# Kernel tuning notes

Hardware: AMD Instinct MI355X
Metric: run time of the kernel (lower is better)

Reference implementation:

```python
import jax, jax.numpy as jnp
import numpy as np

N, NFEAT, NHID, NHID2 = 10000, 512, 256, 128


def setup_inputs() -> dict:
    key = jax.random.key(0)
    k1, k2, k3, k4 = jax.random.split(key, 4)
    x = jax.random.normal(k1, (N, NFEAT), dtype=jnp.float32)
    # sparse-ish row-normalized adjacency, stored dense (as the module's spmm operand)
    raw = jax.random.uniform(k2, (N, N), dtype=jnp.float32)
    adj = jnp.where(raw > 0.995, raw, 0.0)
    adj = adj / jnp.maximum(adj.sum(axis=1, keepdims=True), 1e-6)
    W1 = jax.random.normal(k3, (NFEAT, NHID), dtype=jnp.float32) / np.sqrt(NFEAT)
    b1 = jnp.zeros((NHID,), dtype=jnp.float32)
    W2 = jax.random.normal(k4, (NHID, NHID2), dtype=jnp.float32) / np.sqrt(NHID)
    b2 = jnp.zeros((NHID2,), dtype=jnp.float32)
    return {"x": x, "adj": adj, "W1": W1, "b1": b1, "W2": W2, "b2": b2}


def gcn_conv(x, adj, W, b):
    # standard Kipf GCNConv: adj @ (x @ W) + b
    return adj @ (x @ W) + b


def reference(x, adj, W1, b1, W2, b2):
    h = jax.nn.relu(gcn_conv(x, adj, W1, b1))
    # dropout is identity in inference mode (training=False)
    h = jax.nn.relu(gcn_conv(h, adj, W2, b2))
    return h
```

## Files before the change

### kernel.cpp

```cpp
#include <hip/hip_runtime.h>

#define N_NODES 10000
#define NFEAT   512
#define NHID    256
#define NHID2   128
#define CAP     128

typedef __attribute__((ext_vector_type(8))) short bf16x8;
typedef __attribute__((ext_vector_type(4))) float f32x4;
typedef __attribute__((ext_vector_type(2))) int   i32x2;

__device__ __forceinline__ ushort f2bf(float f){
  union { float f; unsigned u; } v; v.f = f;
  unsigned r = v.u + 0x7FFFu + ((v.u >> 16) & 1u);
  return (ushort)(r >> 16);
}
__device__ __forceinline__ float bf2f(ushort u){
  union { unsigned u; float f; } v; v.u = ((unsigned)u) << 16; return v.f;
}

__global__ void k_cvt(const float* __restrict__ x, const float* __restrict__ W1,
                      const float* __restrict__ W2, ushort* __restrict__ xb,
                      ushort* __restrict__ w1t, ushort* __restrict__ w2t){
  const int b = blockIdx.x, t = threadIdx.x;
  if (b < 5000){
    int i = (b * 256 + t) * 4;
    float4 q = *(const float4*)(x + i);
    ushort4 o; o.x = f2bf(q.x); o.y = f2bf(q.y); o.z = f2bf(q.z); o.w = f2bf(q.w);
    *(ushort4*)(xb + i) = o;
  } else if (b < 5512){
    int id = (b - 5000) * 256 + t;
    int n = id >> 9, k = id & 511;
    w1t[id] = f2bf(W1[k * NHID + n]);
  } else {
    int id = (b - 5512) * 256 + t;
    int n = id >> 8, k = id & 255;
    w2t[id] = f2bf(W2[k * NHID2 + n]);
  }
}

__launch_bounds__(256)
__global__ void k_scan_gemm1(const float* __restrict__ adj, const ushort* __restrict__ xb,
                             const ushort* __restrict__ w1t, ushort* __restrict__ xw1_lo,
                             ushort* __restrict__ xw1_hi, int* __restrict__ row_nnz,
                             i32x2* __restrict__ pja){
  const int b = blockIdx.x, t = threadIdx.x;
  const int lane = t & 63, w = t >> 6;

  if (b < 628){
    const int bx = b % 157, by = b / 157;
    const int wr = w >> 1, wc = w & 1;
    const int r16 = lane & 15, kg = lane >> 4;
    const int row0 = bx * 64 + wr * 32;
    const int col0 = by * 64 + wc * 32;

    int arow[2], bcol[2];
    #pragma unroll
    for (int r = 0; r < 2; r++){
      int ar = row0 + r * 16 + r16;
      arow[r] = (ar >= N_NODES) ? (N_NODES - 1) : ar;
    }
    #pragma unroll
    for (int c = 0; c < 2; c++) bcol[c] = col0 + c * 16 + r16;

    f32x4 acc[2][2];
    #pragma unroll
    for (int r = 0; r < 2; r++)
      #pragma unroll
      for (int c = 0; c < 2; c++)
        acc[r][c] = (f32x4){0.f, 0.f, 0.f, 0.f};

    bf16x8 aA[2], bA[2], aB[2], bB[2];
    auto LOADF = [&](bf16x8* a, bf16x8* bb, int k0){
      #pragma unroll
      for (int r = 0; r < 2; r++)
        a[r] = *(const bf16x8*)(xb + (size_t)arow[r] * NFEAT + k0 + kg * 8);
      #pragma unroll
      for (int c = 0; c < 2; c++)
        bb[c] = *(const bf16x8*)(w1t + (size_t)bcol[c] * NFEAT + k0 + kg * 8);
    };
    auto MM = [&](bf16x8* a, bf16x8* bb){
      #pragma unroll
      for (int r = 0; r < 2; r++)
        #pragma unroll
        for (int c = 0; c < 2; c++)
          acc[r][c] = __builtin_amdgcn_mfma_f32_16x16x32_bf16(a[r], bb[c], acc[r][c], 0, 0, 0);
    };

    LOADF(aA, bA, 0);
    #pragma unroll
    for (int k0 = 0; k0 < NFEAT; k0 += 64){
      if (k0 + 32 < NFEAT) LOADF(aB, bB, k0 + 32);
      MM(aA, bA);
      if (k0 + 64 < NFEAT) LOADF(aA, bA, k0 + 64);
      if (k0 + 32 < NFEAT) MM(aB, bB);
    }

    ushort* dst = (by < 2) ? xw1_lo : xw1_hi;
    const int cbase = (by < 2) ? 0 : 128;
    #pragma unroll
    for (int r = 0; r < 2; r++)
      #pragma unroll
      for (int c = 0; c < 2; c++){
        int col = col0 + c * 16 + r16 - cbase;
        #pragma unroll
        for (int i = 0; i < 4; i++){
          int row = row0 + r * 16 + kg * 4 + i;
          if (row < N_NODES) dst[(size_t)row * 128 + col] = f2bf(acc[r][c][i]);
        }
      }
    return;
  }

  const int r = b - 628;
  const float* row = adj + (size_t)r * N_NODES;
  __shared__ int swave[4];

  f32x4 vals[10];
  #pragma unroll
  for (int v = 0; v < 9; v++)
    vals[v] = __builtin_nontemporal_load((const f32x4*)(row + v * 1024 + t * 4));
  vals[9] = (f32x4){0.f, 0.f, 0.f, 0.f};
  if (t < 196) vals[9] = __builtin_nontemporal_load((const f32x4*)(row + 9216 + t * 4));

  int cnt = 0;
  #pragma unroll
  for (int v = 0; v < 10; v++)
    cnt += (vals[v].x != 0.f) + (vals[v].y != 0.f) + (vals[v].z != 0.f) + (vals[v].w != 0.f);

  int incl = cnt;
  #pragma unroll
  for (int d = 1; d < 64; d <<= 1){
    int u = __shfl_up(incl, d, 64);
    if (lane >= d) incl += u;
  }
  if (lane == 63) swave[w] = incl;
  __syncthreads();
  int woff = 0, total = 0;
  #pragma unroll
  for (int i = 0; i < 4; i++){
    int s = swave[i];
    total += s;
    if (i < w) woff += s;
  }
  int pos = woff + incl - cnt;

  #pragma unroll
  for (int v = 0; v < 10; v++){
    float q[4] = {vals[v].x, vals[v].y, vals[v].z, vals[v].w};
    #pragma unroll
    for (int e = 0; e < 4; e++){
      if (q[e] != 0.f && pos < CAP){
        pja[(size_t)r * CAP + pos] = (i32x2){(v * 1024 + t * 4 + e) << 8, __float_as_int(q[e])};
        pos++;
      }
    }
  }
  if (t == 0) row_nnz[r] = min(total, CAP);
}

__launch_bounds__(256)
__global__ void k_agg1(const int* __restrict__ row_nnz, const i32x2* __restrict__ pja,
                       const ushort* __restrict__ xw1_lo, const ushort* __restrict__ xw1_hi,
                       const float* __restrict__ b1, ushort* __restrict__ Hb){
  const int half = blockIdx.x & 1;
  const int r0   = (blockIdx.x >> 1) * 16;
  const int t = threadIdx.x;
  __shared__ i32x2 sl[16][CAP];
  __shared__ int   sn[16];
  if (t < 16) sn[t] = row_nnz[r0 + t];
  #pragma unroll
  for (int e = 0; e < 8; e++){
    int idx = t + e * 256;
    int rr = idx >> 7, kk = idx & (CAP - 1);
    sl[rr][kk] = pja[(size_t)(r0 + rr) * CAP + kk];
  }
  __syncthreads();

  const int wv = t >> 6, lane = t & 63;
  const char* table = (const char*)(half ? xw1_hi : xw1_lo);
  const float bias0 = b1[half * 128 + lane * 2 + 0];
  const float bias1 = b1[half * 128 + lane * 2 + 1];

  #pragma unroll
  for (int rr = wv; rr < 16; rr += 4){
    const int n = sn[rr];
    float a0 = 0.f, a1 = 0.f;
    for (int k = 0; k < n; k++){
      i32x2 p = sl[rr][k];
      uint pk = *(const uint*)(table + p.x + lane * 4);
      float a = __int_as_float(p.y);
      a0 += a * bf2f((ushort)(pk & 0xffff));
      a1 += a * bf2f((ushort)(pk >> 16));
    }
    uint o = ((uint)f2bf(fmaxf(a1 + bias1, 0.f)) << 16) | (uint)f2bf(fmaxf(a0 + bias0, 0.f));
    *(uint*)(Hb + (size_t)(r0 + rr) * NHID + half * 128 + lane * 2) = o;
  }
}

__launch_bounds__(256)
__global__ void k_gemm2(const ushort* __restrict__ A, const ushort* __restrict__ Bt,
                        ushort* __restrict__ C){
  const int lane = threadIdx.x & 63;
  const int w    = threadIdx.x >> 6;
  const int wr   = w >> 1, wc = w & 1;
  const int r16  = lane & 15;
  const int kg   = lane >> 4;
  const int row0 = blockIdx.x * 64 + wr * 32;
  const int col0 = blockIdx.y * 64 + wc * 32;

  int arow[2], bcol[2];
  #pragma unroll
  for (int r = 0; r < 2; r++){
    int ar = row0 + r * 16 + r16;
    arow[r] = (ar >= N_NODES) ? (N_NODES - 1) : ar;
  }
  #pragma unroll
  for (int c = 0; c < 2; c++) bcol[c] = col0 + c * 16 + r16;

  f32x4 acc[2][2];
  #pragma unroll
  for (int r = 0; r < 2; r++)
    #pragma unroll
    for (int c = 0; c < 2; c++)
      acc[r][c] = (f32x4){0.f, 0.f, 0.f, 0.f};

  bf16x8 aA[2], bA[2], aB[2], bB[2];
  auto LOADF = [&](bf16x8* a, bf16x8* bb, int k0){
    #pragma unroll
    for (int r = 0; r < 2; r++)
      a[r] = *(const bf16x8*)(A + (size_t)arow[r] * NHID + k0 + kg * 8);
    #pragma unroll
    for (int c = 0; c < 2; c++)
      bb[c] = *(const bf16x8*)(Bt + (size_t)bcol[c] * NHID + k0 + kg * 8);
  };
  auto MM = [&](bf16x8* a, bf16x8* bb){
    #pragma unroll
    for (int r = 0; r < 2; r++)
      #pragma unroll
      for (int c = 0; c < 2; c++)
        acc[r][c] = __builtin_amdgcn_mfma_f32_16x16x32_bf16(a[r], bb[c], acc[r][c], 0, 0, 0);
  };

  LOADF(aA, bA, 0);
  #pragma unroll
  for (int k0 = 0; k0 < NHID; k0 += 64){
    if (k0 + 32 < NHID) LOADF(aB, bB, k0 + 32);
    MM(aA, bA);
    if (k0 + 64 < NHID) LOADF(aA, bA, k0 + 64);
    if (k0 + 32 < NHID) MM(aB, bB);
  }

  #pragma unroll
  for (int r = 0; r < 2; r++)
    #pragma unroll
    for (int c = 0; c < 2; c++){
      int col = col0 + c * 16 + r16;
      #pragma unroll
      for (int i = 0; i < 4; i++){
        int row = row0 + r * 16 + kg * 4 + i;
        if (row < N_NODES) C[(size_t)row * NHID2 + col] = f2bf(acc[r][c][i]);
      }
    }
}

__launch_bounds__(256)
__global__ void k_agg2(const int* __restrict__ row_nnz, const i32x2* __restrict__ pja,
                       const ushort* __restrict__ hw2b, const float* __restrict__ b2,
                       float* __restrict__ out){
  const int r0 = blockIdx.x * 8;
  const int t = threadIdx.x;
  __shared__ i32x2 sl[8][CAP];
  __shared__ int   sn[8];
  if (t < 8) sn[t] = row_nnz[r0 + t];
  #pragma unroll
  for (int e = 0; e < 4; e++){
    int idx = t + e * 256;
    int rr = idx >> 7, kk = idx & (CAP - 1);
    sl[rr][kk] = pja[(size_t)(r0 + rr) * CAP + kk];
  }
  __syncthreads();

  const int wv = t >> 6, lane = t & 63;
  const char* table = (const char*)hw2b;
  const float bias0 = b2[lane * 2 + 0];
  const float bias1 = b2[lane * 2 + 1];

  #pragma unroll
  for (int rr = wv; rr < 8; rr += 4){
    const int n = sn[rr];
    float a0 = 0.f, a1 = 0.f;
    for (int k = 0; k < n; k++){
      i32x2 p = sl[rr][k];
      uint pk = *(const uint*)(table + p.x + lane * 4);
      float a = __int_as_float(p.y);
      a0 += a * bf2f((ushort)(pk & 0xffff));
      a1 += a * bf2f((ushort)(pk >> 16));
    }
    float2 o = make_float2(fmaxf(a0 + bias0, 0.f), fmaxf(a1 + bias1, 0.f));
    *(float2*)(out + (size_t)(r0 + rr) * NHID2 + lane * 2) = o;
  }
}

extern "C" void kernel_launch(void* const* d_in, const int* in_sizes, int n_in,
                              void* d_out, int out_size, void* d_ws, size_t ws_size,
                              hipStream_t stream){
  const float* x   = (const float*)d_in[0];
  const float* adj = (const float*)d_in[1];
  const float* W1  = (const float*)d_in[2];
  const float* b1  = (const float*)d_in[3];
  const float* W2  = (const float*)d_in[4];
  const float* b2  = (const float*)d_in[5];
  float* out = (float*)d_out;
  char*  ws  = (char*)d_ws;

  ushort* xb     = (ushort*)(ws);
  ushort* w1t    = (ushort*)(ws + 10240000);
  ushort* w2t    = (ushort*)(ws + 10502144);
  ushort* xw1_lo = (ushort*)(ws + 10567680);
  ushort* xw1_hi = (ushort*)(ws + 13127680);
  ushort* Hb     = (ushort*)(ws + 15687680);
  ushort* hw2b   = (ushort*)(ws + 20807680);
  int*    nnz    = (int*)(ws + 23367680);
  i32x2*  pja    = (i32x2*)(ws + 23407680);

  k_cvt<<<5640, 256, 0, stream>>>(x, W1, W2, xb, w1t, w2t);

  k_scan_gemm1<<<10628, 256, 0, stream>>>(adj, xb, w1t, xw1_lo, xw1_hi, nnz, pja);

  k_agg1<<<1250, 256, 0, stream>>>(nnz, pja, xw1_lo, xw1_hi, b1, Hb);

  k_gemm2<<<dim3(157, 2), 256, 0, stream>>>(Hb, w2t, hw2b);

  k_agg2<<<1250, 256, 0, stream>>>(nnz, pja, hw2b, b2, out);
}
```

Before: 142.3 us.

## Split adjacency row scan into half-row blocks with padded per-half neighbor lists

The scan kernel now processes each adjacency row as two 5000-column halves in separate blocks, doubling the block count and halving the registers each thread holds. Each half writes up to 64 entries into its own slot, and the unused entries are zero-filled. The aggregation kernels then walk both half-lists together with an unrolled loop over a padded count, which exposes more independent gathers. The GEMM loops drop the manual double buffering in favour of a simple unroll-4 loop. This adds zero-padding writes and some wasted gathers, and caps each half at 64 neighbors.

```diff
diff --git a/kernel.cpp b/kernel.cpp
--- a/kernel.cpp
+++ b/kernel.cpp
@@ -42,7 +42,7 @@
 __launch_bounds__(256)
 __global__ void k_scan_gemm1(const float* __restrict__ adj, const ushort* __restrict__ xb,
                              const ushort* __restrict__ w1t, ushort* __restrict__ xw1_lo,
-                             ushort* __restrict__ xw1_hi, int* __restrict__ row_nnz,
+                             ushort* __restrict__ xw1_hi, int* __restrict__ nnzh,
                              i32x2* __restrict__ pja){
   const int b = blockIdx.x, t = threadIdx.x;
   const int lane = t & 63, w = t >> 6;
@@ -70,30 +70,20 @@
       for (int c = 0; c < 2; c++)
         acc[r][c] = (f32x4){0.f, 0.f, 0.f, 0.f};
 
-    bf16x8 aA[2], bA[2], aB[2], bB[2];
-    auto LOADF = [&](bf16x8* a, bf16x8* bb, int k0){
+    #pragma unroll 4
+    for (int k0 = 0; k0 < NFEAT; k0 += 32){
+      bf16x8 a[2], bb[2];
       #pragma unroll
       for (int r = 0; r < 2; r++)
         a[r] = *(const bf16x8*)(xb + (size_t)arow[r] * NFEAT + k0 + kg * 8);
       #pragma unroll
       for (int c = 0; c < 2; c++)
         bb[c] = *(const bf16x8*)(w1t + (size_t)bcol[c] * NFEAT + k0 + kg * 8);
-    };
-    auto MM = [&](bf16x8* a, bf16x8* bb){
       #pragma unroll
       for (int r = 0; r < 2; r++)
         #pragma unroll
         for (int c = 0; c < 2; c++)
           acc[r][c] = __builtin_amdgcn_mfma_f32_16x16x32_bf16(a[r], bb[c], acc[r][c], 0, 0, 0);
-    };
-
-    LOADF(aA, bA, 0);
-    #pragma unroll
-    for (int k0 = 0; k0 < NFEAT; k0 += 64){
-      if (k0 + 32 < NFEAT) LOADF(aB, bB, k0 + 32);
-      MM(aA, bA);
-      if (k0 + 64 < NFEAT) LOADF(aA, bA, k0 + 64);
-      if (k0 + 32 < NFEAT) MM(aB, bB);
     }
 
     ushort* dst = (by < 2) ? xw1_lo : xw1_hi;
@@ -112,20 +102,21 @@
     return;
   }
 
-  const int r = b - 628;
-  const float* row = adj + (size_t)r * N_NODES;
+  const int s = b - 628;
+  const int r = s >> 1, half = s & 1;
+  const float* row = adj + (size_t)r * N_NODES + half * 5000;
   __shared__ int swave[4];
 
-  f32x4 vals[10];
-  #pragma unroll
-  for (int v = 0; v < 9; v++)
+  f32x4 vals[5];
+  #pragma unroll
+  for (int v = 0; v < 4; v++)
     vals[v] = __builtin_nontemporal_load((const f32x4*)(row + v * 1024 + t * 4));
-  vals[9] = (f32x4){0.f, 0.f, 0.f, 0.f};
-  if (t < 196) vals[9] = __builtin_nontemporal_load((const f32x4*)(row + 9216 + t * 4));
+  vals[4] = (f32x4){0.f, 0.f, 0.f, 0.f};
+  if (t < 226) vals[4] = __builtin_nontemporal_load((const f32x4*)(row + 4096 + t * 4));
 
   int cnt = 0;
   #pragma unroll
-  for (int v = 0; v < 10; v++)
+  for (int v = 0; v < 5; v++)
     cnt += (vals[v].x != 0.f) + (vals[v].y != 0.f) + (vals[v].z != 0.f) + (vals[v].w != 0.f);
 
   int incl = cnt;
@@ -139,36 +130,41 @@
   int woff = 0, total = 0;
   #pragma unroll
   for (int i = 0; i < 4; i++){
-    int s = swave[i];
-    total += s;
-    if (i < w) woff += s;
+    int sv = swave[i];
+    total += sv;
+    if (i < w) woff += sv;
   }
   int pos = woff + incl - cnt;
 
-  #pragma unroll
-  for (int v = 0; v < 10; v++){
+  const size_t slot0 = (size_t)r * CAP + half * 64;
+  const int jbase = half * 5000;
+  #pragma unroll
+  for (int v = 0; v < 5; v++){
     float q[4] = {vals[v].x, vals[v].y, vals[v].z, vals[v].w};
+    int ebase = jbase + ((v < 4) ? (v * 1024 + t * 4) : (4096 + t * 4));
     #pragma unroll
     for (int e = 0; e < 4; e++){
-      if (q[e] != 0.f && pos < CAP){
-        pja[(size_t)r * CAP + pos] = (i32x2){(v * 1024 + t * 4 + e) << 8, __float_as_int(q[e])};
+      if (q[e] != 0.f && pos < 64){
+        pja[slot0 + pos] = (i32x2){(ebase + e) << 8, __float_as_int(q[e])};
         pos++;
       }
     }
   }
-  if (t == 0) row_nnz[r] = min(total, CAP);
+  for (int z = total + t; z < 64; z += 256)
+    pja[slot0 + z] = (i32x2){0, 0};
+  if (t == 0) nnzh[s] = min(total, 64);
 }
 
 __launch_bounds__(256)
-__global__ void k_agg1(const int* __restrict__ row_nnz, const i32x2* __restrict__ pja,
+__global__ void k_agg1(const int* __restrict__ nnzh, const i32x2* __restrict__ pja,
                        const ushort* __restrict__ xw1_lo, const ushort* __restrict__ xw1_hi,
                        const float* __restrict__ b1, ushort* __restrict__ Hb){
   const int half = blockIdx.x & 1;
   const int r0   = (blockIdx.x >> 1) * 16;
   const int t = threadIdx.x;
   __shared__ i32x2 sl[16][CAP];
-  __shared__ int   sn[16];
-  if (t < 16) sn[t] = row_nnz[r0 + t];
+  __shared__ int   sn[32];
+  if (t < 32) sn[t] = nnzh[r0 * 2 + t];
   #pragma unroll
   for (int e = 0; e < 8; e++){
     int idx = t + e * 256;
@@ -184,14 +180,23 @@
 
   #pragma unroll
   for (int rr = wv; rr < 16; rr += 4){
-    const int n = sn[rr];
+    const int n0 = sn[rr * 2], n1 = sn[rr * 2 + 1];
+    const int mp = (max(n0, n1) + 3) & ~3;
     float a0 = 0.f, a1 = 0.f;
-    for (int k = 0; k < n; k++){
-      i32x2 p = sl[rr][k];
-      uint pk = *(const uint*)(table + p.x + lane * 4);
-      float a = __int_as_float(p.y);
-      a0 += a * bf2f((ushort)(pk & 0xffff));
-      a1 += a * bf2f((ushort)(pk >> 16));
+    for (int k = 0; k < mp; k += 2){
+      #pragma unroll
+      for (int u = 0; u < 2; u++){
+        i32x2 p = sl[rr][k + u];
+        uint pk = *(const uint*)(table + p.x + lane * 4);
+        float a = __int_as_float(p.y);
+        a0 += a * bf2f((ushort)(pk & 0xffff));
+        a1 += a * bf2f((ushort)(pk >> 16));
+        i32x2 p2 = sl[rr][64 + k + u];
+        uint pk2 = *(const uint*)(table + p2.x + lane * 4);
+        float a2 = __int_as_float(p2.y);
+        a0 += a2 * bf2f((ushort)(pk2 & 0xffff));
+        a1 += a2 * bf2f((ushort)(pk2 >> 16));
+      }
     }
     uint o = ((uint)f2bf(fmaxf(a1 + bias1, 0.f)) << 16) | (uint)f2bf(fmaxf(a0 + bias0, 0.f));
     *(uint*)(Hb + (size_t)(r0 + rr) * NHID + half * 128 + lane * 2) = o;
@@ -225,30 +230,20 @@
     for (int c = 0; c < 2; c++)
       acc[r][c] = (f32x4){0.f, 0.f, 0.f, 0.f};
 
-  bf16x8 aA[2], bA[2], aB[2], bB[2];
-  auto LOADF = [&](bf16x8* a, bf16x8* bb, int k0){
+  #pragma unroll 4
+  for (int k0 = 0; k0 < NHID; k0 += 32){
+    bf16x8 a[2], bb[2];
     #pragma unroll
     for (int r = 0; r < 2; r++)
       a[r] = *(const bf16x8*)(A + (size_t)arow[r] * NHID + k0 + kg * 8);
     #pragma unroll
     for (int c = 0; c < 2; c++)
       bb[c] = *(const bf16x8*)(Bt + (size_t)bcol[c] * NHID + k0 + kg * 8);
-  };
-  auto MM = [&](bf16x8* a, bf16x8* bb){
     #pragma unroll
     for (int r = 0; r < 2; r++)
       #pragma unroll
       for (int c = 0; c < 2; c++)
         acc[r][c] = __builtin_amdgcn_mfma_f32_16x16x32_bf16(a[r], bb[c], acc[r][c], 0, 0, 0);
-  };
-
-  LOADF(aA, bA, 0);
-  #pragma unroll
-  for (int k0 = 0; k0 < NHID; k0 += 64){
-    if (k0 + 32 < NHID) LOADF(aB, bB, k0 + 32);
-    MM(aA, bA);
-    if (k0 + 64 < NHID) LOADF(aA, bA, k0 + 64);
-    if (k0 + 32 < NHID) MM(aB, bB);
   }
 
   #pragma unroll
@@ -265,14 +260,14 @@
 }
 
 __launch_bounds__(256)
-__global__ void k_agg2(const int* __restrict__ row_nnz, const i32x2* __restrict__ pja,
+__global__ void k_agg2(const int* __restrict__ nnzh, const i32x2* __restrict__ pja,
                        const ushort* __restrict__ hw2b, const float* __restrict__ b2,
                        float* __restrict__ out){
   const int r0 = blockIdx.x * 8;
   const int t = threadIdx.x;
   __shared__ i32x2 sl[8][CAP];
-  __shared__ int   sn[8];
-  if (t < 8) sn[t] = row_nnz[r0 + t];
+  __shared__ int   sn[16];
+  if (t < 16) sn[t] = nnzh[r0 * 2 + t];
   #pragma unroll
   for (int e = 0; e < 4; e++){
     int idx = t + e * 256;
@@ -288,14 +283,23 @@
 
   #pragma unroll
   for (int rr = wv; rr < 8; rr += 4){
-    const int n = sn[rr];
+    const int n0 = sn[rr * 2], n1 = sn[rr * 2 + 1];
+    const int mp = (max(n0, n1) + 3) & ~3;
     float a0 = 0.f, a1 = 0.f;
-    for (int k = 0; k < n; k++){
-      i32x2 p = sl[rr][k];
-      uint pk = *(const uint*)(table + p.x + lane * 4);
-      float a = __int_as_float(p.y);
-      a0 += a * bf2f((ushort)(pk & 0xffff));
-      a1 += a * bf2f((ushort)(pk >> 16));
+    for (int k = 0; k < mp; k += 2){
+      #pragma unroll
+      for (int u = 0; u < 2; u++){
+        i32x2 p = sl[rr][k + u];
+        uint pk = *(const uint*)(table + p.x + lane * 4);
+        float a = __int_as_float(p.y);
+        a0 += a * bf2f((ushort)(pk & 0xffff));
+        a1 += a * bf2f((ushort)(pk >> 16));
+        i32x2 p2 = sl[rr][64 + k + u];
+        uint pk2 = *(const uint*)(table + p2.x + lane * 4);
+        float a2 = __int_as_float(p2.y);
+        a0 += a2 * bf2f((ushort)(pk2 & 0xffff));
+        a1 += a2 * bf2f((ushort)(pk2 >> 16));
+      }
     }
     float2 o = make_float2(fmaxf(a0 + bias0, 0.f), fmaxf(a1 + bias1, 0.f));
     *(float2*)(out + (size_t)(r0 + rr) * NHID2 + lane * 2) = o;
@@ -321,16 +325,16 @@
   ushort* xw1_hi = (ushort*)(ws + 13127680);
   ushort* Hb     = (ushort*)(ws + 15687680);
   ushort* hw2b   = (ushort*)(ws + 20807680);
-  int*    nnz    = (int*)(ws + 23367680);
-  i32x2*  pja    = (i32x2*)(ws + 23407680);
+  int*    nnzh   = (int*)(ws + 23367680);
+  i32x2*  pja    = (i32x2*)(ws + 23447680);
 
   k_cvt<<<5640, 256, 0, stream>>>(x, W1, W2, xb, w1t, w2t);
 
-  k_scan_gemm1<<<10628, 256, 0, stream>>>(adj, xb, w1t, xw1_lo, xw1_hi, nnz, pja);
-
-  k_agg1<<<1250, 256, 0, stream>>>(nnz, pja, xw1_lo, xw1_hi, b1, Hb);
+  k_scan_gemm1<<<20628, 256, 0, stream>>>(adj, xb, w1t, xw1_lo, xw1_hi, nnzh, pja);
+
+  k_agg1<<<1250, 256, 0, stream>>>(nnzh, pja, xw1_lo, xw1_hi, b1, Hb);
 
   k_gemm2<<<dim3(157, 2), 256, 0, stream>>>(Hb, w2t, hw2b);
 
-  k_agg2<<<1250, 256, 0, stream>>>(nnz, pja, hw2b, b2, out);
-}
+  k_agg2<<<1250, 256, 0, stream>>>(nnzh, pja, hw2b, b2, out);
+}
```

New measurement: 150.0 us. 5.4% more time.

## Fold fp32-to-bf16 conversion into GEMMs, drop convert kernel, interleave scan and GEMM blocks

Applied to the files above, without the earlier changes.

Removes the separate conversion kernel. Both GEMMs now read fp32 x, W1 and W2 directly and convert to bf16 in registers, with the weights read with a stride down each column instead of from a pre-transposed copy. GEMM tiles in the fused scan+GEMM launch are spread evenly among the adjacency-scan blocks (one in every 17) instead of being launched first, which should overlap compute with the scan's memory traffic. This saves a launch and the xb round trip. The cost is more global traffic per tile, strided uncoalesced weight loads, and the loss of the double-buffered load pipeline.

```diff
diff --git a/kernel.cpp b/kernel.cpp
--- a/kernel.cpp
+++ b/kernel.cpp
@@ -19,36 +19,21 @@
   union { unsigned u; float f; } v; v.u = ((unsigned)u) << 16; return v.f;
 }
 
-__global__ void k_cvt(const float* __restrict__ x, const float* __restrict__ W1,
-                      const float* __restrict__ W2, ushort* __restrict__ xb,
-                      ushort* __restrict__ w1t, ushort* __restrict__ w2t){
-  const int b = blockIdx.x, t = threadIdx.x;
-  if (b < 5000){
-    int i = (b * 256 + t) * 4;
-    float4 q = *(const float4*)(x + i);
-    ushort4 o; o.x = f2bf(q.x); o.y = f2bf(q.y); o.z = f2bf(q.z); o.w = f2bf(q.w);
-    *(ushort4*)(xb + i) = o;
-  } else if (b < 5512){
-    int id = (b - 5000) * 256 + t;
-    int n = id >> 9, k = id & 511;
-    w1t[id] = f2bf(W1[k * NHID + n]);
-  } else {
-    int id = (b - 5512) * 256 + t;
-    int n = id >> 8, k = id & 255;
-    w2t[id] = f2bf(W2[k * NHID2 + n]);
-  }
-}
-
 __launch_bounds__(256)
-__global__ void k_scan_gemm1(const float* __restrict__ adj, const ushort* __restrict__ xb,
-                             const ushort* __restrict__ w1t, ushort* __restrict__ xw1_lo,
+__global__ void k_scan_gemm1(const float* __restrict__ adj, const float* __restrict__ x,
+                             const float* __restrict__ W1, ushort* __restrict__ xw1_lo,
                              ushort* __restrict__ xw1_hi, int* __restrict__ row_nnz,
                              i32x2* __restrict__ pja){
   const int b = blockIdx.x, t = threadIdx.x;
   const int lane = t & 63, w = t >> 6;
 
-  if (b < 628){
-    const int bx = b % 157, by = b / 157;
+  int gid = -1, sid = -1;
+  if (b >= 10625)            gid = 625 + (b - 10625);
+  else if ((b % 17) == 16)   gid = b / 17;
+  else                       sid = b - b / 17;
+
+  if (gid >= 0){
+    const int bx = gid % 157, by = gid / 157;
     const int wr = w >> 1, wc = w & 1;
     const int r16 = lane & 15, kg = lane >> 4;
     const int row0 = bx * 64 + wr * 32;
@@ -70,30 +55,27 @@
       for (int c = 0; c < 2; c++)
         acc[r][c] = (f32x4){0.f, 0.f, 0.f, 0.f};
 
-    bf16x8 aA[2], bA[2], aB[2], bB[2];
-    auto LOADF = [&](bf16x8* a, bf16x8* bb, int k0){
-      #pragma unroll
-      for (int r = 0; r < 2; r++)
-        a[r] = *(const bf16x8*)(xb + (size_t)arow[r] * NFEAT + k0 + kg * 8);
-      #pragma unroll
-      for (int c = 0; c < 2; c++)
-        bb[c] = *(const bf16x8*)(w1t + (size_t)bcol[c] * NFEAT + k0 + kg * 8);
-    };
-    auto MM = [&](bf16x8* a, bf16x8* bb){
+    for (int k0 = 0; k0 < NFEAT; k0 += 32){
+      bf16x8 a[2], bb[2];
+      #pragma unroll
+      for (int r = 0; r < 2; r++){
+        const float* src = x + (size_t)arow[r] * NFEAT + k0 + kg * 8;
+        f32x4 u0 = *(const f32x4*)(src);
+        f32x4 u1 = *(const f32x4*)(src + 4);
+        a[r][0] = f2bf(u0.x); a[r][1] = f2bf(u0.y); a[r][2] = f2bf(u0.z); a[r][3] = f2bf(u0.w);
+        a[r][4] = f2bf(u1.x); a[r][5] = f2bf(u1.y); a[r][6] = f2bf(u1.z); a[r][7] = f2bf(u1.w);
+      }
+      #pragma unroll
+      for (int c = 0; c < 2; c++){
+        const float* src = W1 + (size_t)(k0 + kg * 8) * NHID + bcol[c];
+        #pragma unroll
+        for (int j = 0; j < 8; j++) bb[c][j] = f2bf(src[j * NHID]);
+      }
       #pragma unroll
       for (int r = 0; r < 2; r++)
         #pragma unroll
         for (int c = 0; c < 2; c++)
           acc[r][c] = __builtin_amdgcn_mfma_f32_16x16x32_bf16(a[r], bb[c], acc[r][c], 0, 0, 0);
-    };
-
-    LOADF(aA, bA, 0);
-    #pragma unroll
-    for (int k0 = 0; k0 < NFEAT; k0 += 64){
-      if (k0 + 32 < NFEAT) LOADF(aB, bB, k0 + 32);
-      MM(aA, bA);
-      if (k0 + 64 < NFEAT) LOADF(aA, bA, k0 + 64);
-      if (k0 + 32 < NFEAT) MM(aB, bB);
     }
 
     ushort* dst = (by < 2) ? xw1_lo : xw1_hi;
@@ -112,7 +94,7 @@
     return;
   }
 
-  const int r = b - 628;
+  const int r = sid;
   const float* row = adj + (size_t)r * N_NODES;
   __shared__ int swave[4];
 
@@ -199,7 +181,7 @@
 }
 
 __launch_bounds__(256)
-__global__ void k_gemm2(const ushort* __restrict__ A, const ushort* __restrict__ Bt,
+__global__ void k_gemm2(const ushort* __restrict__ A, const float* __restrict__ W2,
                         ushort* __restrict__ C){
   const int lane = threadIdx.x & 63;
   const int w    = threadIdx.x >> 6;
@@ -225,30 +207,22 @@
     for (int c = 0; c < 2; c++)
       acc[r][c] = (f32x4){0.f, 0.f, 0.f, 0.f};
 
-  bf16x8 aA[2], bA[2], aB[2], bB[2];
-  auto LOADF = [&](bf16x8* a, bf16x8* bb, int k0){
+  for (int k0 = 0; k0 < NHID; k0 += 32){
+    bf16x8 a[2], bb[2];
     #pragma unroll
     for (int r = 0; r < 2; r++)
       a[r] = *(const bf16x8*)(A + (size_t)arow[r] * NHID + k0 + kg * 8);
     #pragma unroll
-    for (int c = 0; c < 2; c++)
-      bb[c] = *(const bf16x8*)(Bt + (size_t)bcol[c] * NHID + k0 + kg * 8);
-  };
-  auto MM = [&](bf16x8* a, bf16x8* bb){
+    for (int c = 0; c < 2; c++){
+      const float* src = W2 + (size_t)(k0 + kg * 8) * NHID2 + bcol[c];
+      #pragma unroll
+      for (int j = 0; j < 8; j++) bb[c][j] = f2bf(src[j * NHID2]);
+    }
     #pragma unroll
     for (int r = 0; r < 2; r++)
       #pragma unroll
       for (int c = 0; c < 2; c++)
         acc[r][c] = __builtin_amdgcn_mfma_f32_16x16x32_bf16(a[r], bb[c], acc[r][c], 0, 0, 0);
-  };
-
-  LOADF(aA, bA, 0);
-  #pragma unroll
-  for (int k0 = 0; k0 < NHID; k0 += 64){
-    if (k0 + 32 < NHID) LOADF(aB, bB, k0 + 32);
-    MM(aA, bA);
-    if (k0 + 64 < NHID) LOADF(aA, bA, k0 + 64);
-    if (k0 + 32 < NHID) MM(aB, bB);
   }
 
   #pragma unroll
@@ -314,23 +288,18 @@
   float* out = (float*)d_out;
   char*  ws  = (char*)d_ws;
 
-  ushort* xb     = (ushort*)(ws);
-  ushort* w1t    = (ushort*)(ws + 10240000);
-  ushort* w2t    = (ushort*)(ws + 10502144);
-  ushort* xw1_lo = (ushort*)(ws + 10567680);
-  ushort* xw1_hi = (ushort*)(ws + 13127680);
-  ushort* Hb     = (ushort*)(ws + 15687680);
-  ushort* hw2b   = (ushort*)(ws + 20807680);
-  int*    nnz    = (int*)(ws + 23367680);
-  i32x2*  pja    = (i32x2*)(ws + 23407680);
-
-  k_cvt<<<5640, 256, 0, stream>>>(x, W1, W2, xb, w1t, w2t);
-
-  k_scan_gemm1<<<10628, 256, 0, stream>>>(adj, xb, w1t, xw1_lo, xw1_hi, nnz, pja);
+  ushort* xw1_lo = (ushort*)(ws);
+  ushort* xw1_hi = (ushort*)(ws +  2560000);
+  ushort* Hb     = (ushort*)(ws +  5120000);
+  ushort* hw2b   = (ushort*)(ws + 10240000);
+  int*    nnz    = (int*)(ws + 12800000);
+  i32x2*  pja    = (i32x2*)(ws + 12840000);
+
+  k_scan_gemm1<<<10628, 256, 0, stream>>>(adj, x, W1, xw1_lo, xw1_hi, nnz, pja);
 
   k_agg1<<<1250, 256, 0, stream>>>(nnz, pja, xw1_lo, xw1_hi, b1, Hb);
 
-  k_gemm2<<<dim3(157, 2), 256, 0, stream>>>(Hb, w2t, hw2b);
+  k_gemm2<<<dim3(157, 2), 256, 0, stream>>>(Hb, W2, hw2b);
 
   k_agg2<<<1250, 256, 0, stream>>>(nnz, pja, hw2b, b2, out);
 }
```

Result: slower. 145.6 us (+2.3%).

## Fuse bf16 conversion into adjacency scan kernel and split GEMM1 into its own launch

Applied to the files above, without the earlier changes.

Moves the x/W1/W2 bf16 conversion blocks into the adjacency-scan kernel, placed after the 10000 scan blocks. GEMM1 becomes a separate launch after that kernel instead of sharing a launch with the scan. The scan now overlaps with the conversion rather than with GEMM1, and the standalone conversion launch is removed. The cost is that GEMM1 no longer hides behind the bandwidth-bound scan and now runs serially as its own launch.

```diff
diff --git a/kernel.cpp b/kernel.cpp
--- a/kernel.cpp
+++ b/kernel.cpp
@@ -19,100 +19,34 @@
   union { unsigned u; float f; } v; v.u = ((unsigned)u) << 16; return v.f;
 }
 
-__global__ void k_cvt(const float* __restrict__ x, const float* __restrict__ W1,
-                      const float* __restrict__ W2, ushort* __restrict__ xb,
-                      ushort* __restrict__ w1t, ushort* __restrict__ w2t){
+__launch_bounds__(256)
+__global__ void k_scan_cvt(const float* __restrict__ adj, const float* __restrict__ x,
+                           const float* __restrict__ W1, const float* __restrict__ W2,
+                           ushort* __restrict__ xb, ushort* __restrict__ w1t,
+                           ushort* __restrict__ w2t, int* __restrict__ row_nnz,
+                           i32x2* __restrict__ pja){
   const int b = blockIdx.x, t = threadIdx.x;
-  if (b < 5000){
-    int i = (b * 256 + t) * 4;
-    float4 q = *(const float4*)(x + i);
-    ushort4 o; o.x = f2bf(q.x); o.y = f2bf(q.y); o.z = f2bf(q.z); o.w = f2bf(q.w);
-    *(ushort4*)(xb + i) = o;
-  } else if (b < 5512){
-    int id = (b - 5000) * 256 + t;
-    int n = id >> 9, k = id & 511;
-    w1t[id] = f2bf(W1[k * NHID + n]);
-  } else {
-    int id = (b - 5512) * 256 + t;
-    int n = id >> 8, k = id & 255;
-    w2t[id] = f2bf(W2[k * NHID2 + n]);
-  }
-}
-
-__launch_bounds__(256)
-__global__ void k_scan_gemm1(const float* __restrict__ adj, const ushort* __restrict__ xb,
-                             const ushort* __restrict__ w1t, ushort* __restrict__ xw1_lo,
-                             ushort* __restrict__ xw1_hi, int* __restrict__ row_nnz,
-                             i32x2* __restrict__ pja){
-  const int b = blockIdx.x, t = threadIdx.x;
+
+  if (b >= N_NODES){
+    if (b < 15000){
+      int i = ((b - N_NODES) * 256 + t) * 4;
+      float4 q = *(const float4*)(x + i);
+      ushort4 o; o.x = f2bf(q.x); o.y = f2bf(q.y); o.z = f2bf(q.z); o.w = f2bf(q.w);
+      *(ushort4*)(xb + i) = o;
+    } else if (b < 15512){
+      int id = (b - 15000) * 256 + t;
+      int n = id >> 9, k = id & 511;
+      w1t[id] = f2bf(W1[k * NHID + n]);
+    } else {
+      int id = (b - 15512) * 256 + t;
+      int n = id >> 8, k = id & 255;
+      w2t[id] = f2bf(W2[k * NHID2 + n]);
+    }
+    return;
+  }
+
+  const int r = b;
   const int lane = t & 63, w = t >> 6;
-
-  if (b < 628){
-    const int bx = b % 157, by = b / 157;
-    const int wr = w >> 1, wc = w & 1;
-    const int r16 = lane & 15, kg = lane >> 4;
-    const int row0 = bx * 64 + wr * 32;
-    const int col0 = by * 64 + wc * 32;
-
-    int arow[2], bcol[2];
-    #pragma unroll
-    for (int r = 0; r < 2; r++){
-      int ar = row0 + r * 16 + r16;
-      arow[r] = (ar >= N_NODES) ? (N_NODES - 1) : ar;
-    }
-    #pragma unroll
-    for (int c = 0; c < 2; c++) bcol[c] = col0 + c * 16 + r16;
-
-    f32x4 acc[2][2];
-    #pragma unroll
-    for (int r = 0; r < 2; r++)
-      #pragma unroll
-      for (int c = 0; c < 2; c++)
-        acc[r][c] = (f32x4){0.f, 0.f, 0.f, 0.f};
-
-    bf16x8 aA[2], bA[2], aB[2], bB[2];
-    auto LOADF = [&](bf16x8* a, bf16x8* bb, int k0){
-      #pragma unroll
-      for (int r = 0; r < 2; r++)
-        a[r] = *(const bf16x8*)(xb + (size_t)arow[r] * NFEAT + k0 + kg * 8);
-      #pragma unroll
-      for (int c = 0; c < 2; c++)
-        bb[c] = *(const bf16x8*)(w1t + (size_t)bcol[c] * NFEAT + k0 + kg * 8);
-    };
-    auto MM = [&](bf16x8* a, bf16x8* bb){
-      #pragma unroll
-      for (int r = 0; r < 2; r++)
-        #pragma unroll
-        for (int c = 0; c < 2; c++)
-          acc[r][c] = __builtin_amdgcn_mfma_f32_16x16x32_bf16(a[r], bb[c], acc[r][c], 0, 0, 0);
-    };
-
-    LOADF(aA, bA, 0);
-    #pragma unroll
-    for (int k0 = 0; k0 < NFEAT; k0 += 64){
-      if (k0 + 32 < NFEAT) LOADF(aB, bB, k0 + 32);
-      MM(aA, bA);
-      if (k0 + 64 < NFEAT) LOADF(aA, bA, k0 + 64);
-      if (k0 + 32 < NFEAT) MM(aB, bB);
-    }
-
-    ushort* dst = (by < 2) ? xw1_lo : xw1_hi;
-    const int cbase = (by < 2) ? 0 : 128;
-    #pragma unroll
-    for (int r = 0; r < 2; r++)
-      #pragma unroll
-      for (int c = 0; c < 2; c++){
-        int col = col0 + c * 16 + r16 - cbase;
-        #pragma unroll
-        for (int i = 0; i < 4; i++){
-          int row = row0 + r * 16 + kg * 4 + i;
-          if (row < N_NODES) dst[(size_t)row * 128 + col] = f2bf(acc[r][c][i]);
-        }
-      }
-    return;
-  }
-
-  const int r = b - 628;
   const float* row = adj + (size_t)r * N_NODES;
   __shared__ int swave[4];
 
@@ -157,6 +91,74 @@
     }
   }
   if (t == 0) row_nnz[r] = min(total, CAP);
+}
+
+__launch_bounds__(256)
+__global__ void k_gemm1(const ushort* __restrict__ A, const ushort* __restrict__ Bt,
+                        ushort* __restrict__ xw1_lo, ushort* __restrict__ xw1_hi){
+  const int lane = threadIdx.x & 63;
+  const int w    = threadIdx.x >> 6;
+  const int wr   = w >> 1, wc = w & 1;
+  const int r16  = lane & 15;
+  const int kg   = lane >> 4;
+  const int row0 = blockIdx.x * 64 + wr * 32;
+  const int col0 = blockIdx.y * 64 + wc * 32;
+
+  int arow[2], bcol[2];
+  #pragma unroll
+  for (int r = 0; r < 2; r++){
+    int ar = row0 + r * 16 + r16;
+    arow[r] = (ar >= N_NODES) ? (N_NODES - 1) : ar;
+  }
+  #pragma unroll
+  for (int c = 0; c < 2; c++) bcol[c] = col0 + c * 16 + r16;
+
+  f32x4 acc[2][2];
+  #pragma unroll
+  for (int r = 0; r < 2; r++)
+    #pragma unroll
+    for (int c = 0; c < 2; c++)
+      acc[r][c] = (f32x4){0.f, 0.f, 0.f, 0.f};
+
+  bf16x8 aA[2], bA[2], aB[2], bB[2];
+  auto LOADF = [&](bf16x8* a, bf16x8* bb, int k0){
+    #pragma unroll
+    for (int r = 0; r < 2; r++)
+      a[r] = *(const bf16x8*)(A + (size_t)arow[r] * NFEAT + k0 + kg * 8);
+    #pragma unroll
+    for (int c = 0; c < 2; c++)
+      bb[c] = *(const bf16x8*)(Bt + (size_t)bcol[c] * NFEAT + k0 + kg * 8);
+  };
+  auto MM = [&](bf16x8* a, bf16x8* bb){
+    #pragma unroll
+    for (int r = 0; r < 2; r++)
+      #pragma unroll
+      for (int c = 0; c < 2; c++)
+        acc[r][c] = __builtin_amdgcn_mfma_f32_16x16x32_bf16(a[r], bb[c], acc[r][c], 0, 0, 0);
+  };
+
+  LOADF(aA, bA, 0);
+  #pragma unroll
+  for (int k0 = 0; k0 < NFEAT; k0 += 64){
+    if (k0 + 32 < NFEAT) LOADF(aB, bB, k0 + 32);
+    MM(aA, bA);
+    if (k0 + 64 < NFEAT) LOADF(aA, bA, k0 + 64);
+    if (k0 + 32 < NFEAT) MM(aB, bB);
+  }
+
+  ushort* dst = (blockIdx.y < 2) ? xw1_lo : xw1_hi;
+  const int cbase = (blockIdx.y < 2) ? 0 : 128;
+  #pragma unroll
+  for (int r = 0; r < 2; r++)
+    #pragma unroll
+    for (int c = 0; c < 2; c++){
+      int col = col0 + c * 16 + r16 - cbase;
+      #pragma unroll
+      for (int i = 0; i < 4; i++){
+        int row = row0 + r * 16 + kg * 4 + i;
+        if (row < N_NODES) dst[(size_t)row * 128 + col] = f2bf(acc[r][c][i]);
+      }
+    }
 }
 
 __launch_bounds__(256)
@@ -324,9 +326,9 @@
   int*    nnz    = (int*)(ws + 23367680);
   i32x2*  pja    = (i32x2*)(ws + 23407680);
 
-  k_cvt<<<5640, 256, 0, stream>>>(x, W1, W2, xb, w1t, w2t);
-
-  k_scan_gemm1<<<10628, 256, 0, stream>>>(adj, xb, w1t, xw1_lo, xw1_hi, nnz, pja);
+  k_scan_cvt<<<15640, 256, 0, stream>>>(adj, x, W1, W2, xb, w1t, w2t, nnz, pja);
+
+  k_gemm1<<<dim3(157, 4), 256, 0, stream>>>(xb, w1t, xw1_lo, xw1_hi);
 
   k_agg1<<<1250, 256, 0, stream>>>(nnz, pja, xw1_lo, xw1_hi, b1, Hb);
 
```

Measured after the change: 142.0 us, median of 2. No clear change (-0.3%).
